# Optimization experiments

Measured on AMD Instinct MI355X. Metric: run time of the kernel, lower is better.

## Reference

```python
import jax, jax.numpy as jnp
import numpy as np

GRID = 7            # n_cells
P = 2               # predictions_per_cell
NC = 20             # n_classes
N = GRID * GRID * P # 98 candidate boxes
INPUT = 448.0
CELL = 64.0         # input_size / n_cells
K = 10              # max_n_objects
CONF_THR = 0.1
NMS_THR = 0.7


def setup_inputs() -> dict:
    key = jax.random.key(0)
    ks = jax.random.split(key, 7)
    B = 256
    return {
        "x": jax.random.normal(ks[0], (B, 1280, 14, 14), dtype=jnp.float32),
        "conv_w": jax.random.normal(ks[1], (128, 1280), dtype=jnp.float32) * 0.02,
        "conv_b": jnp.zeros((128,), dtype=jnp.float32),
        "fc1_w": jax.random.normal(ks[2], (4096, 6272), dtype=jnp.float32) * 0.01,
        "fc1_b": jnp.zeros((4096,), dtype=jnp.float32),
        "fc2_w": jax.random.normal(ks[3], (1470, 4096), dtype=jnp.float32) * 0.01,
        "fc2_b": jnp.zeros((1470,), dtype=jnp.float32),
    }


def _pairwise_iou(b):
    # b: [N, 4] corner boxes
    x1, y1, x2, y2 = b[:, 0], b[:, 1], b[:, 2], b[:, 3]
    area = jnp.maximum(x2 - x1, 0.0) * jnp.maximum(y2 - y1, 0.0)
    ix1 = jnp.maximum(x1[:, None], x1[None, :])
    iy1 = jnp.maximum(y1[:, None], y1[None, :])
    ix2 = jnp.minimum(x2[:, None], x2[None, :])
    iy2 = jnp.minimum(y2[:, None], y2[None, :])
    inter = jnp.maximum(ix2 - ix1, 0.0) * jnp.maximum(iy2 - iy1, 0.0)
    union = area[:, None] + area[None, :] - inter
    return jnp.where(union > 0.0, inter / union, 0.0)


def _nms_single(boxes, conf, labels):
    # boxes [N,4], conf [N], labels [N] int. Greedy NMS with fixed shapes.
    order = jnp.argsort(-conf)
    b, c, l = boxes[order], conf[order], labels[order]
    keep0 = c > CONF_THR            # confidence thresholding before NMS
    iou = _pairwise_iou(b)          # [N,N], N=98 (small)
    idx = jnp.arange(N)

    def body(i, keep):
        sup = (iou[i] > NMS_THR) & keep[i] & (idx > i)
        return keep & ~sup

    keep = jax.lax.fori_loop(0, N, body, keep0)
    score = jnp.where(keep, c, -1.0)
    topv, topi = jax.lax.top_k(score, K)   # top max_n_objects survivors
    valid = topv > CONF_THR
    bb = jnp.where(valid[:, None], b[topi], 0.0)   # pad with zeros
    cc = jnp.where(valid, c[topi], 0.0)
    ll = jnp.where(valid, l[topi], 0)
    return bb, ll, cc


def _decode(x, conv_w, conv_b, fc1_w, fc1_b, fc2_w, fc2_b):
    B = x.shape[0]
    # 1x1 conv, stride 2: [B,1280,14,14] -> [B,128,7,7]
    h = x[:, :, ::2, ::2]
    h = jnp.einsum("bchw,oc->bohw", h, conv_w) + conv_b[None, :, None, None]
    h = h.reshape(B, -1)                       # channel-major flatten, like torch
    h = h @ fc1_w.T + fc1_b
    h = jnp.where(h >= 0, h, 0.1 * h)          # leaky_relu(0.1); dropout is identity in eval
    h = h @ fc2_w.T + fc2_b
    h = jax.nn.sigmoid(h)
    xywh = h[:, : N * 4].reshape(B, GRID, GRID, P, 4)
    conf = h[:, N * 4 : N * 5].reshape(B, GRID, GRID, P)
    cls = h[:, N * 5 :].reshape(B, GRID, GRID, NC)
    # decode to absolute corner boxes (xywh_to_boxes)
    offs = jnp.arange(GRID, dtype=h.dtype) * CELL
    cx = xywh[..., 0] * CELL + offs[None, :, None, None]   # offset i on first grid axis -> x
    cy = xywh[..., 1] * CELL + offs[None, None, :, None]   # offset j on second grid axis -> y
    w = xywh[..., 2] * INPUT
    hh = xywh[..., 3] * INPUT
    x1 = jnp.clip(cx - 0.5 * w, 0.0, INPUT)
    y1 = jnp.clip(cy - 0.5 * hh, 0.0, INPUT)
    x2 = jnp.clip(cx + 0.5 * w, 0.0, INPUT)
    y2 = jnp.clip(cy + 0.5 * hh, 0.0, INPUT)
    boxes = jnp.stack([x1, y1, x2, y2], axis=-1).reshape(B, N, 4)
    conf = conf.reshape(B, N)
    cls_pred = jnp.broadcast_to(cls[:, :, :, None, :], (B, GRID, GRID, P, NC)).reshape(B, N, NC)
    labels = jnp.argmax(cls_pred, axis=2)
    return boxes, conf, labels


def reference(x, conv_w, conv_b, fc1_w, fc1_b, fc2_w, fc2_b):
    boxes, conf, labels = _decode(x, conv_w, conv_b, fc1_w, fc1_b, fc2_w, fc2_b)
    all_boxes, all_labels, all_confs = jax.vmap(_nms_single)(boxes, conf, labels)
    return all_boxes, all_labels, all_confs
```

## Files before the change

kernel.cpp:

```cpp
#include <hip/hip_runtime.h>
#include <math.h>

#define BATCH 256
#define CIN 1280
#define COUT 128
#define F1IN 6272
#define F1OUT 4096
#define F2OUT 1470
#define NBOX 98

__global__ __launch_bounds__(256) void conv_kernel(const float* __restrict__ x,
                                                   const float* __restrict__ w,
                                                   const float* __restrict__ bias,
                                                   double* __restrict__ h1) {
    const int b = blockIdx.x;
    const int obase = blockIdx.y * 32;
    const int tid = threadIdx.x;
    const int o_l = tid & 31;
    const int g = tid >> 5;

    __shared__ double xs[64 * 49];
    __shared__ float wT[64 * 33];

    double acc[7];
#pragma unroll
    for (int k = 0; k < 7; ++k) acc[k] = 0.0;

    const float* xb = x + (size_t)b * CIN * 196;

    for (int cb = 0; cb < CIN; cb += 64) {
        __syncthreads();
        for (int idx = tid; idx < 64 * 49; idx += 256) {
            int c = idx / 49, s = idx - c * 49;
            int si = s / 7, sj = s - si * 7;
            xs[idx] = (double)xb[(size_t)(cb + c) * 196 + si * 28 + sj * 2];
        }
        for (int idx = tid; idx < 64 * 32; idx += 256) {
            int o = idx >> 6, c = idx & 63;
            wT[c * 33 + o] = w[(size_t)(obase + o) * CIN + cb + c];
        }
        __syncthreads();
        for (int c = 0; c < 64; ++c) {
            double wv = (double)wT[c * 33 + o_l];
#pragma unroll
            for (int k = 0; k < 7; ++k) {
                int sg = g + 8 * k;
                if (sg < 49) acc[k] = fma(wv, xs[c * 49 + sg], acc[k]);
            }
        }
    }

    const int o = obase + o_l;
    const double bv = (double)bias[o];
    for (int k = 0; k < 7; ++k) {
        int sg = g + 8 * k;
        if (sg < 49) h1[(size_t)b * F1IN + (size_t)o * 49 + sg] = acc[k] + bv;
    }
}

template <bool NCHECK, bool AFUSE>
__global__ __launch_bounds__(256) void fc_splitk_kernel(const double* __restrict__ A,
                                                        const float* __restrict__ W,
                                                        const float* __restrict__ abias,
                                                        double* __restrict__ C,
                                                        int N, int K, int kchunks_per_slice) {
    __shared__ double As2[16][66];
    __shared__ double Ws2[16][66];

    const int mbase = blockIdx.x * 64;
    const int nbase = blockIdx.y * 64;
    const int kb0 = blockIdx.z * kchunks_per_slice * 16;
    const int kb1 = kb0 + kchunks_per_slice * 16;
    const int tid = threadIdx.x;
    const int tm = tid >> 4;
    const int tn = tid & 15;

    double acc[4][4];
#pragma unroll
    for (int i = 0; i < 4; ++i)
#pragma unroll
        for (int j = 0; j < 4; ++j) acc[i][j] = 0.0;

    for (int kb = kb0; kb < kb1; kb += 16) {
        __syncthreads();
        for (int idx = tid; idx < 64 * 16; idx += 256) {
            int r = idx >> 4, kk = idx & 15;
            double v = A[(size_t)(mbase + r) * K + kb + kk];
            if (AFUSE) {
                v += (double)abias[kb + kk];
                v = (v >= 0.0) ? v : 0.1 * v;
            }
            As2[kk][r] = v;
        }
        for (int idx = tid; idx < 64 * 16; idx += 256) {
            int c = idx >> 4, kk = idx & 15;
            int n = nbase + c;
            Ws2[kk][c] = (!NCHECK || n < N) ? (double)W[(size_t)n * K + kb + kk] : 0.0;
        }
        __syncthreads();
        for (int kk = 0; kk < 16; ++kk) {
            double a[4];
            double bw[4];
#pragma unroll
            for (int i = 0; i < 4; ++i) a[i] = As2[kk][tm + 16 * i];
#pragma unroll
            for (int j = 0; j < 4; ++j) bw[j] = Ws2[kk][tn + 16 * j];
#pragma unroll
            for (int i = 0; i < 4; ++i)
#pragma unroll
                for (int j = 0; j < 4; ++j)
                    acc[i][j] = fma(a[i], bw[j], acc[i][j]);
        }
    }

#pragma unroll
    for (int i = 0; i < 4; ++i) {
        int m = mbase + tm + 16 * i;
#pragma unroll
        for (int j = 0; j < 4; ++j) {
            int n = nbase + tn + 16 * j;
            if (!NCHECK || n < N)
                atomicAdd(&C[(size_t)m * N + n], acc[i][j]);
        }
    }
}

__global__ __launch_bounds__(128) void decode_nms_kernel(const double* __restrict__ Z,
                                                         const float* __restrict__ fc2b,
                                                         float* __restrict__ out_boxes,
                                                         float* __restrict__ out_labels,
                                                         float* __restrict__ out_confs) {
    const int b = blockIdx.x;
    const int tid = threadIdx.x;

    __shared__ double sAll[F2OUT];
    __shared__ double bx[NBOX][4];
    __shared__ double cf[NBOX];
    __shared__ int lab[NBOX];
    __shared__ double sbx[NBOX][4];
    __shared__ double scf[NBOX];
    __shared__ int slab[NBOX];
    __shared__ unsigned long long suprow[NBOX][2];

    const double* z = Z + (size_t)b * F2OUT;
    for (int i = tid; i < F2OUT; i += 128) {
        double v = z[i] + (double)fc2b[i];
        sAll[i] = 1.0 / (1.0 + exp(-v));
    }
    __syncthreads();

    for (int n = tid; n < NBOX; n += 128) {
        int gi = n / 14;
        int gj = (n % 14) >> 1;
        double cx = sAll[4 * n + 0] * 64.0 + 64.0 * (double)gi;
        double cy = sAll[4 * n + 1] * 64.0 + 64.0 * (double)gj;
        double w  = sAll[4 * n + 2] * 448.0;
        double hh = sAll[4 * n + 3] * 448.0;
        double x1 = cx - 0.5 * w,  y1 = cy - 0.5 * hh;
        double x2 = cx + 0.5 * w,  y2 = cy + 0.5 * hh;
        x1 = x1 < 0.0 ? 0.0 : (x1 > 448.0 ? 448.0 : x1);
        y1 = y1 < 0.0 ? 0.0 : (y1 > 448.0 ? 448.0 : y1);
        x2 = x2 < 0.0 ? 0.0 : (x2 > 448.0 ? 448.0 : x2);
        y2 = y2 < 0.0 ? 0.0 : (y2 > 448.0 ? 448.0 : y2);
        bx[n][0] = x1; bx[n][1] = y1; bx[n][2] = x2; bx[n][3] = y2;
        cf[n] = sAll[392 + n];
        int cell = n >> 1;
        double best = sAll[490 + cell * 20];
        int bl = 0;
        for (int c = 1; c < 20; ++c) {
            double v = sAll[490 + cell * 20 + c];
            if (v > best) { best = v; bl = c; }
        }
        lab[n] = bl;
    }
    __syncthreads();

    for (int n = tid; n < NBOX; n += 128) {
        double cn = cf[n];
        int r = 0;
        for (int m = 0; m < NBOX; ++m) {
            double cm = cf[m];
            if (cm > cn || (cm == cn && m < n)) ++r;
        }
        scf[r] = cn;
        slab[r] = lab[n];
        sbx[r][0] = bx[n][0]; sbx[r][1] = bx[n][1];
        sbx[r][2] = bx[n][2]; sbx[r][3] = bx[n][3];
    }
    __syncthreads();

    for (int i = tid; i < NBOX; i += 128) {
        double x1 = sbx[i][0], y1 = sbx[i][1], x2 = sbx[i][2], y2 = sbx[i][3];
        double ai = fmax(x2 - x1, 0.0) * fmax(y2 - y1, 0.0);
        unsigned long long m0 = 0ull, m1 = 0ull;
        for (int j = 0; j < NBOX; ++j) {
            double jx1 = sbx[j][0], jy1 = sbx[j][1], jx2 = sbx[j][2], jy2 = sbx[j][3];
            double xx1 = fmax(x1, jx1), yy1 = fmax(y1, jy1);
            double xx2 = fmin(x2, jx2), yy2 = fmin(y2, jy2);
            double inter = fmax(xx2 - xx1, 0.0) * fmax(yy2 - yy1, 0.0);
            double aj = fmax(jx2 - jx1, 0.0) * fmax(jy2 - jy1, 0.0);
            double uni = ai + aj - inter;
            double iou = (uni > 0.0) ? inter / uni : 0.0;
            if (iou > 0.7) {
                if (j < 64) m0 |= 1ull << j;
                else        m1 |= 1ull << (j - 64);
            }
        }
        suprow[i][0] = m0;
        suprow[i][1] = m1;
    }
    __syncthreads();

    if (tid == 0) {
        unsigned long long k0 = 0ull, k1 = 0ull;
        for (int i = 0; i < NBOX; ++i) {
            if (scf[i] > 0.1) {
                if (i < 64) k0 |= 1ull << i;
                else        k1 |= 1ull << (i - 64);
            }
        }
        for (int i = 0; i < NBOX; ++i) {
            bool ki = (i < 64) ? ((k0 >> i) & 1ull) : ((k1 >> (i - 64)) & 1ull);
            if (!ki) continue;
            unsigned long long g0, g1;
            if (i < 63)       { g0 = (~0ull) << (i + 1); g1 = ~0ull; }
            else if (i == 63) { g0 = 0ull;               g1 = ~0ull; }
            else              { g0 = 0ull;               g1 = (~0ull) << (i - 63); }
            k0 &= ~(suprow[i][0] & g0);
            k1 &= ~(suprow[i][1] & g1);
        }
        int cnt = 0;
        for (int i = 0; i < NBOX && cnt < 10; ++i) {
            bool ki = (i < 64) ? ((k0 >> i) & 1ull) : ((k1 >> (i - 64)) & 1ull);
            if (!ki) continue;
            out_boxes[(size_t)b * 40 + cnt * 4 + 0] = (float)sbx[i][0];
            out_boxes[(size_t)b * 40 + cnt * 4 + 1] = (float)sbx[i][1];
            out_boxes[(size_t)b * 40 + cnt * 4 + 2] = (float)sbx[i][2];
            out_boxes[(size_t)b * 40 + cnt * 4 + 3] = (float)sbx[i][3];
            out_labels[b * 10 + cnt] = (float)slab[i];
            out_confs[b * 10 + cnt]  = (float)scf[i];
            ++cnt;
        }
        for (; cnt < 10; ++cnt) {
            out_boxes[(size_t)b * 40 + cnt * 4 + 0] = 0.0f;
            out_boxes[(size_t)b * 40 + cnt * 4 + 1] = 0.0f;
            out_boxes[(size_t)b * 40 + cnt * 4 + 2] = 0.0f;
            out_boxes[(size_t)b * 40 + cnt * 4 + 3] = 0.0f;
            out_labels[b * 10 + cnt] = 0.0f;
            out_confs[b * 10 + cnt]  = 0.0f;
        }
    }
}

extern "C" void kernel_launch(void* const* d_in, const int* in_sizes, int n_in,
                              void* d_out, int out_size, void* d_ws, size_t ws_size,
                              hipStream_t stream) {
    const float* x      = (const float*)d_in[0];
    const float* conv_w = (const float*)d_in[1];
    const float* conv_b = (const float*)d_in[2];
    const float* fc1_w  = (const float*)d_in[3];
    const float* fc1_b  = (const float*)d_in[4];
    const float* fc2_w  = (const float*)d_in[5];
    const float* fc2_b  = (const float*)d_in[6];

    double* h1 = (double*)d_ws;
    double* a1 = h1 + (size_t)BATCH * F1IN;
    double* a2 = a1 + (size_t)BATCH * F1OUT;

    float* out_boxes  = (float*)d_out;
    float* out_labels = out_boxes + (size_t)BATCH * 40;
    float* out_confs  = out_labels + (size_t)BATCH * 10;

    hipMemsetAsync(a1, 0, (size_t)BATCH * F1OUT * sizeof(double), stream);
    hipMemsetAsync(a2, 0, (size_t)BATCH * F2OUT * sizeof(double), stream);

    conv_kernel<<<dim3(BATCH, 4), 256, 0, stream>>>(x, conv_w, conv_b, h1);

    fc_splitk_kernel<false, false><<<dim3(4, 64, 8), 256, 0, stream>>>(h1, fc1_w, nullptr, a1, F1OUT, F1IN, 49);

    fc_splitk_kernel<true, true><<<dim3(4, 23, 16), 256, 0, stream>>>(a1, fc2_w, fc1_b, a2, F2OUT, F1OUT, 16);

    decode_nms_kernel<<<BATCH, 128, 0, stream>>>(a2, fc2_b, out_boxes, out_labels, out_confs);
}
```

Measured before the change: 1.462 ms.

## Recast strided conv as tiled GEMM and enlarge FC M-tile to 128 rows

The 1x1 stride-2 conv is rewritten as a 64x64 register-tiled GEMM over (out-channel, batch*spatial), gathering the strided input directly into shared memory. This replaces the per-image kernel that reloaded the weights for every batch element. The FC split-K kernels now use 128-row M tiles with 8x4 accumulators per thread, so each weight tile is reused across twice as many rows. The cost is higher register pressure, more shared memory and half as many blocks, which may reduce occupancy.

```diff
diff --git a/kernel.cpp b/kernel.cpp
--- a/kernel.cpp
+++ b/kernel.cpp
@@ -9,52 +9,76 @@
 #define F2OUT 1470
 #define NBOX 98
 
-__global__ __launch_bounds__(256) void conv_kernel(const float* __restrict__ x,
-                                                   const float* __restrict__ w,
-                                                   const float* __restrict__ bias,
-                                                   double* __restrict__ h1) {
-    const int b = blockIdx.x;
-    const int obase = blockIdx.y * 32;
+__global__ __launch_bounds__(256) void conv_gemm_kernel(const float* __restrict__ wA,
+                                                        const float* __restrict__ x,
+                                                        const float* __restrict__ bias,
+                                                        double* __restrict__ h1) {
+    __shared__ double As2[16][66];
+    __shared__ double Ws2[16][66];
+
+    const int mbase = blockIdx.x * 64;
+    const int nbase = blockIdx.y * 64;
     const int tid = threadIdx.x;
-    const int o_l = tid & 31;
-    const int g = tid >> 5;
-
-    __shared__ double xs[64 * 49];
-    __shared__ float wT[64 * 33];
-
-    double acc[7];
-#pragma unroll
-    for (int k = 0; k < 7; ++k) acc[k] = 0.0;
-
-    const float* xb = x + (size_t)b * CIN * 196;
-
-    for (int cb = 0; cb < CIN; cb += 64) {
+    const int tm = tid >> 4;
+    const int tn = tid & 15;
+
+    const int scol = tid & 63;
+    const int sn = nbase + scol;
+    const int sb = sn / 49;
+    const int ss = sn - 49 * sb;
+    const int ssi = ss / 7;
+    const int ssj = ss - 7 * ssi;
+    const size_t soff = (size_t)sb * (CIN * 196) + ssi * 28 + ssj * 2;
+
+    double acc[4][4];
+#pragma unroll
+    for (int i = 0; i < 4; ++i)
+#pragma unroll
+        for (int j = 0; j < 4; ++j) acc[i][j] = 0.0;
+
+    for (int cb = 0; cb < CIN; cb += 16) {
         __syncthreads();
-        for (int idx = tid; idx < 64 * 49; idx += 256) {
-            int c = idx / 49, s = idx - c * 49;
-            int si = s / 7, sj = s - si * 7;
-            xs[idx] = (double)xb[(size_t)(cb + c) * 196 + si * 28 + sj * 2];
-        }
-        for (int idx = tid; idx < 64 * 32; idx += 256) {
-            int o = idx >> 6, c = idx & 63;
-            wT[c * 33 + o] = w[(size_t)(obase + o) * CIN + cb + c];
+        for (int idx = tid; idx < 64 * 16; idx += 256) {
+            int r = idx >> 4, kk = idx & 15;
+            As2[kk][r] = (double)wA[(size_t)(mbase + r) * CIN + cb + kk];
+        }
+        {
+            int kk = tid >> 6;
+#pragma unroll
+            for (int it = 0; it < 4; ++it, kk += 4)
+                Ws2[kk][scol] = (double)x[soff + (size_t)(cb + kk) * 196];
         }
         __syncthreads();
-        for (int c = 0; c < 64; ++c) {
-            double wv = (double)wT[c * 33 + o_l];
-#pragma unroll
-            for (int k = 0; k < 7; ++k) {
-                int sg = g + 8 * k;
-                if (sg < 49) acc[k] = fma(wv, xs[c * 49 + sg], acc[k]);
-            }
-        }
-    }
-
-    const int o = obase + o_l;
-    const double bv = (double)bias[o];
-    for (int k = 0; k < 7; ++k) {
-        int sg = g + 8 * k;
-        if (sg < 49) h1[(size_t)b * F1IN + (size_t)o * 49 + sg] = acc[k] + bv;
+        for (int kk = 0; kk < 16; ++kk) {
+            double a[4];
+            double bw[4];
+#pragma unroll
+            for (int i = 0; i < 4; ++i) a[i] = As2[kk][tm + 16 * i];
+#pragma unroll
+            for (int j = 0; j < 4; ++j) bw[j] = Ws2[kk][tn + 16 * j];
+#pragma unroll
+            for (int i = 0; i < 4; ++i)
+#pragma unroll
+                for (int j = 0; j < 4; ++j)
+                    acc[i][j] = fma(a[i], bw[j], acc[i][j]);
+        }
+    }
+
+    int outoff[4];
+#pragma unroll
+    for (int j = 0; j < 4; ++j) {
+        int n = nbase + tn + 16 * j;
+        int b = n / 49;
+        int s = n - 49 * b;
+        outoff[j] = b * F1IN + s;
+    }
+#pragma unroll
+    for (int i = 0; i < 4; ++i) {
+        int m = mbase + tm + 16 * i;
+        double bv = (double)bias[m];
+#pragma unroll
+        for (int j = 0; j < 4; ++j)
+            h1[(size_t)outoff[j] + (size_t)m * 49] = acc[i][j] + bv;
     }
 }
 
@@ -64,10 +88,10 @@
                                                         const float* __restrict__ abias,
                                                         double* __restrict__ C,
                                                         int N, int K, int kchunks_per_slice) {
-    __shared__ double As2[16][66];
+    __shared__ double As2[16][130];
     __shared__ double Ws2[16][66];
 
-    const int mbase = blockIdx.x * 64;
+    const int mbase = blockIdx.x * 128;
     const int nbase = blockIdx.y * 64;
     const int kb0 = blockIdx.z * kchunks_per_slice * 16;
     const int kb1 = kb0 + kchunks_per_slice * 16;
@@ -75,15 +99,15 @@
     const int tm = tid >> 4;
     const int tn = tid & 15;
 
-    double acc[4][4];
-#pragma unroll
-    for (int i = 0; i < 4; ++i)
+    double acc[8][4];
+#pragma unroll
+    for (int i = 0; i < 8; ++i)
 #pragma unroll
         for (int j = 0; j < 4; ++j) acc[i][j] = 0.0;
 
     for (int kb = kb0; kb < kb1; kb += 16) {
         __syncthreads();
-        for (int idx = tid; idx < 64 * 16; idx += 256) {
+        for (int idx = tid; idx < 128 * 16; idx += 256) {
             int r = idx >> 4, kk = idx & 15;
             double v = A[(size_t)(mbase + r) * K + kb + kk];
             if (AFUSE) {
@@ -99,14 +123,14 @@
         }
         __syncthreads();
         for (int kk = 0; kk < 16; ++kk) {
-            double a[4];
+            double a[8];
             double bw[4];
 #pragma unroll
-            for (int i = 0; i < 4; ++i) a[i] = As2[kk][tm + 16 * i];
+            for (int i = 0; i < 8; ++i) a[i] = As2[kk][tm + 16 * i];
 #pragma unroll
             for (int j = 0; j < 4; ++j) bw[j] = Ws2[kk][tn + 16 * j];
 #pragma unroll
-            for (int i = 0; i < 4; ++i)
+            for (int i = 0; i < 8; ++i)
 #pragma unroll
                 for (int j = 0; j < 4; ++j)
                     acc[i][j] = fma(a[i], bw[j], acc[i][j]);
@@ -114,7 +138,7 @@
     }
 
 #pragma unroll
-    for (int i = 0; i < 4; ++i) {
+    for (int i = 0; i < 8; ++i) {
         int m = mbase + tm + 16 * i;
 #pragma unroll
         for (int j = 0; j < 4; ++j) {
@@ -274,11 +298,11 @@
     hipMemsetAsync(a1, 0, (size_t)BATCH * F1OUT * sizeof(double), stream);
     hipMemsetAsync(a2, 0, (size_t)BATCH * F2OUT * sizeof(double), stream);
 
-    conv_kernel<<<dim3(BATCH, 4), 256, 0, stream>>>(x, conv_w, conv_b, h1);
-
-    fc_splitk_kernel<false, false><<<dim3(4, 64, 8), 256, 0, stream>>>(h1, fc1_w, nullptr, a1, F1OUT, F1IN, 49);
-
-    fc_splitk_kernel<true, true><<<dim3(4, 23, 16), 256, 0, stream>>>(a1, fc2_w, fc1_b, a2, F2OUT, F1OUT, 16);
+    conv_gemm_kernel<<<dim3(2, 196), 256, 0, stream>>>(conv_w, x, conv_b, h1);
+
+    fc_splitk_kernel<false, false><<<dim3(2, 64, 8), 256, 0, stream>>>(h1, fc1_w, nullptr, a1, F1OUT, F1IN, 49);
+
+    fc_splitk_kernel<true, true><<<dim3(2, 23, 16), 256, 0, stream>>>(a1, fc2_w, fc1_b, a2, F2OUT, F1OUT, 16);
 
     decode_nms_kernel<<<BATCH, 128, 0, stream>>>(a2, fc2_b, out_boxes, out_labels, out_confs);
 }
```

After: 1.187 ms. -18.8%, faster.
